# Optimization experiments

Measured on AMD Instinct MI355X. Metric: run time of the kernel, lower is better.

Reference implementation:

```python
import jax, jax.numpy as jnp
import numpy as np

B, H, W, C = 32, 56, 56, 192
HEADS = 6
WS = 7            # window size
SS = 3            # shift size
N = WS * WS       # tokens per window (49)
HID = 4 * C
EPS = 1e-5


def _rel_index():
    coords = np.stack(np.meshgrid(np.arange(WS), np.arange(WS), indexing='ij')).reshape(2, -1)
    rel = (coords[:, :, None] - coords[:, None, :]).transpose(1, 2, 0)
    rel[:, :, 0] += WS - 1
    rel[:, :, 1] += WS - 1
    rel[:, :, 0] *= 2 * WS - 1
    return rel.sum(-1)  # [N, N] int


def _attn_mask():
    # shift mask, identical to the torch construction; static -> numpy
    m = np.zeros((H, W))
    cnt = 0
    for hs in (slice(0, -WS), slice(-WS, -SS), slice(-SS, None)):
        for ws in (slice(0, -WS), slice(-WS, -SS), slice(-SS, None)):
            m[hs, ws] = cnt
            cnt += 1
    mw = m.reshape(H // WS, WS, W // WS, WS).transpose(0, 2, 1, 3).reshape(-1, N)  # [nW, N]
    diff = mw[:, None, :] - mw[:, :, None]
    return np.where(diff != 0, -100.0, 0.0).astype(np.float32)  # [nW, N, N]

REL_IDX = jnp.asarray(_rel_index())
ATTN_MASK = jnp.asarray(_attn_mask())


def setup_inputs() -> dict:
    key = jax.random.key(0)
    ks = jax.random.split(key, 16)
    s = 0.02
    return {
        'x': jax.random.normal(ks[0], (B, H, W, C), jnp.float32),
        'norm1_g': jnp.ones((C,), jnp.float32),
        'norm1_b': jnp.zeros((C,), jnp.float32),
        'qkv_w': jax.random.normal(ks[1], (C, 3 * C), jnp.float32) * s,
        'qkv_b': jnp.zeros((3 * C,), jnp.float32),
        'proj_w': jax.random.normal(ks[2], (C, C), jnp.float32) * s,
        'proj_b': jnp.zeros((C,), jnp.float32),
        'bias_table': jax.random.normal(ks[3], ((2 * WS - 1) ** 2, HEADS), jnp.float32) * s,
        'norm2_g': jnp.ones((C,), jnp.float32),
        'norm2_b': jnp.zeros((C,), jnp.float32),
        'fc1_w': jax.random.normal(ks[4], (C, HID), jnp.float32) * s,
        'fc1_b': jnp.zeros((HID,), jnp.float32),
        'fc2_w': jax.random.normal(ks[5], (HID, C), jnp.float32) * s,
        'fc2_b': jnp.zeros((C,), jnp.float32),
    }


def _ln(x, g, b):
    mu = jnp.mean(x, -1, keepdims=True)
    var = jnp.var(x, -1, keepdims=True)
    return (x - mu) * jax.lax.rsqrt(var + EPS) * g + b


def _partition(x):
    # [B,H,W,C] -> [B*nW, N, C]
    return x.reshape(B, H // WS, WS, W // WS, WS, C).transpose(0, 1, 3, 2, 4, 5).reshape(-1, N, C)


def _reverse(w):
    # [B*nW, N, C] -> [B,H,W,C]
    return w.reshape(B, H // WS, W // WS, WS, WS, C).transpose(0, 1, 3, 2, 4, 5).reshape(B, H, W, C)


def reference(x, norm1_g, norm1_b, qkv_w, qkv_b, proj_w, proj_b, bias_table,
              norm2_g, norm2_b, fc1_w, fc1_b, fc2_w, fc2_b):
    hd = C // HEADS
    scale = hd ** -0.5
    sc = x
    h = _ln(x, norm1_g, norm1_b)
    h = jnp.roll(h, (-SS, -SS), (1, 2))
    xw = _partition(h)                                  # [B_, N, C]
    B_ = xw.shape[0]
    qkv = (xw @ qkv_w + qkv_b).reshape(B_, N, 3, HEADS, hd).transpose(2, 0, 3, 1, 4)
    q, k, v = qkv[0], qkv[1], qkv[2]                    # [B_, H, N, hd]
    attn = jnp.einsum('bhnd,bhmd->bhnm', q * scale, k)  # [B_, H, N, N]
    bias = bias_table[REL_IDX.reshape(-1)].reshape(N, N, HEADS).transpose(2, 0, 1)
    attn = attn + bias[None]
    nW = (H // WS) * (W // WS)
    attn = attn.reshape(B, nW, HEADS, N, N) + ATTN_MASK[None, :, None]
    attn = jax.nn.softmax(attn.reshape(-1, HEADS, N, N), axis=-1)
    out = jnp.einsum('bhnm,bhmd->bhnd', attn, v).transpose(0, 2, 1, 3).reshape(B_, N, C)
    out = out @ proj_w + proj_b
    h = _reverse(out)
    h = jnp.roll(h, (SS, SS), (1, 2))
    y = sc + h
    m = _ln(y, norm2_g, norm2_b)
    mlp = jax.nn.gelu(m @ fc1_w + fc1_b, approximate=False) @ fc2_w + fc2_b
    return y + mlp
```

## Files before the change

kernel.cpp:

```cpp
#include <hip/hip_runtime.h>
#include <hip/hip_bf16.h>

typedef __hip_bfloat16 bf16;
typedef float f32x4 __attribute__((ext_vector_type(4)));
typedef short bf16x8 __attribute__((ext_vector_type(8)));
typedef short short4v __attribute__((ext_vector_type(4)));
typedef unsigned int u32;

#define NTOK 100352
#define CC 192
#define HIDN 768

__device__ __forceinline__ float b2f(unsigned short u) {
    union { unsigned int u32v; float f; } x; x.u32v = ((unsigned int)u) << 16; return x.f;
}
__device__ __forceinline__ unsigned short f2b(float f) {
    union { float f; unsigned int u; } x; x.f = f;
    unsigned int r = x.u + 0x7FFF + ((x.u >> 16) & 1);
    return (unsigned short)(r >> 16);
}
__device__ __forceinline__ float gelu_f(float x) {
    return x / (1.0f + __expf(-1.702f * x));
}

typedef __attribute__((address_space(1))) const unsigned char gas_u8;
typedef __attribute__((address_space(3))) unsigned char las_u8;
__device__ __forceinline__ void gload_lds16(const void* g, void* l) {
    __builtin_amdgcn_global_load_lds((gas_u8*)g, (las_u8*)l, 16, 0, 0);
}

__global__ void transpose_k(const float* __restrict__ src, bf16* __restrict__ dst, int R, int C) {
    int idx = blockIdx.x * 256 + threadIdx.x;
    if (idx >= R * C) return;
    int r = idx / C, c = idx % C;
    dst[(size_t)c * R + r] = __float2bfloat16(src[idx]);
}

__global__ void bm_k(const float* __restrict__ btab, float* __restrict__ bm) {
    int idx = blockIdx.x * 256 + threadIdx.x;
    if (idx >= 98304) return;
    int reg = idx & 3, lane = (idx >> 2) & 63, tile = (idx >> 8) & 15;
    int rest = idx >> 12, h = rest % 6, cls = rest / 6;
    int mt = tile >> 2, nt = tile & 3;
    int kk = mt * 16 + (lane >> 4) * 4 + reg;
    int q  = nt * 16 + (lane & 15);
    float v;
    if (kk >= 49 || q >= 49) v = -1e9f;
    else {
        int i1 = q / 7, j1 = q % 7, i2 = kk / 7, j2 = kk % 7;
        v = btab[((i1 - i2 + 6) * 13 + (j1 - j2 + 6)) * 6 + h];
        int hb7 = cls >> 1, wb7 = cls & 1;
        int r1 = (hb7 ? (i1 < 4 ? 1 : 2) : 0) * 3 + (wb7 ? (j1 < 4 ? 1 : 2) : 0);
        int r2 = (hb7 ? (i2 < 4 ? 1 : 2) : 0) * 3 + (wb7 ? (j2 < 4 ? 1 : 2) : 0);
        if (r1 != r2) v -= 100.0f;
    }
    bm[idx] = v;
}

template<bool GATHER>
__global__ __launch_bounds__(256) void ln_k(const float* __restrict__ src,
                                            const float* __restrict__ gamma,
                                            const float* __restrict__ beta,
                                            bf16* __restrict__ dst) {
    int wave = threadIdx.x >> 6, lane = threadIdx.x & 63;
    int t = blockIdx.x * 4 + wave;
    size_t srow;
    if (GATHER) {
        int w = t / 49, n = t % 49;
        int b = w >> 6, wl = w & 63, hb = wl >> 3, wb = wl & 7;
        int i = n / 7, j = n % 7;
        int sh = hb * 7 + i + 3; if (sh >= 56) sh -= 56;
        int sw = wb * 7 + j + 3; if (sw >= 56) sw -= 56;
        srow = ((size_t)(b * 56 + sh) * 56 + sw) * CC;
    } else {
        srow = (size_t)t * CC;
    }
    float v[4];
    int c = lane * 4;
    float sum = 0.f, sq = 0.f;
    if (lane < 48) {
        f32x4 d = *(const f32x4*)(src + srow + c);
        #pragma unroll
        for (int q = 0; q < 4; ++q) { v[q] = d[q]; sum += v[q]; sq += v[q] * v[q]; }
    }
    #pragma unroll
    for (int off = 1; off < 64; off <<= 1) { sum += __shfl_xor(sum, off); sq += __shfl_xor(sq, off); }
    float mu = sum * (1.0f / 192.0f);
    float var = sq * (1.0f / 192.0f) - mu * mu;
    float rstd = rsqrtf(var + 1e-5f);
    if (lane < 48) {
        f32x4 gg = *(const f32x4*)(gamma + c);
        f32x4 bb = *(const f32x4*)(beta + c);
        short4v o;
        #pragma unroll
        for (int q = 0; q < 4; ++q) {
            float val = (v[q] - mu) * rstd * gg[q] + bb[q];
            o[q] = (short)f2b(val);
        }
        *(short4v*)(dst + (size_t)t * CC + c) = o;
    }
}

template<int EPI>
__device__ __forceinline__ void epilogue(
    f32x4 (&acc)[4][2], int tm0, int tn0, int w0, int w1, int lane, int N,
    const float* __restrict__ bias, bf16* __restrict__ outb, float* __restrict__ outf,
    const float* __restrict__ xres, const float* __restrict__ yin)
{
    const int r16 = lane & 15, q4 = (lane >> 4) * 4;
    #pragma unroll
    for (int mt = 0; mt < 4; ++mt) {
        int mm = tm0 + w1 * 64 + mt * 16 + r16;
        size_t rowbase;
        if (EPI == 1) {
            int ww = mm / 49, nn = mm % 49;
            int b_ = ww >> 6, wl = ww & 63, hb = wl >> 3, wb = wl & 7;
            int i = nn / 7, j = nn % 7;
            int oh = hb * 7 + i + 3; if (oh >= 56) oh -= 56;
            int ow = wb * 7 + j + 3; if (ow >= 56) ow -= 56;
            rowbase = ((size_t)(b_ * 56 + oh) * 56 + ow) * CC;
        } else {
            rowbase = (size_t)mm * N;
        }
        #pragma unroll
        for (int nt = 0; nt < 2; ++nt) {
            int col = tn0 + w0 * 32 + nt * 16 + q4;
            f32x4 bv = *(const f32x4*)(bias + col);
            f32x4 v;
            #pragma unroll
            for (int r = 0; r < 4; ++r) v[r] = acc[mt][nt][r] + bv[r];
            if (EPI == 1) {
                f32x4 xr = *(const f32x4*)(xres + rowbase + col);
                #pragma unroll
                for (int r = 0; r < 4; ++r) v[r] += xr[r];
                *(f32x4*)(outf + rowbase + col) = v;
            } else if (EPI == 2) {
                short4v o;
                #pragma unroll
                for (int r = 0; r < 4; ++r) o[r] = (short)f2b(gelu_f(v[r]));
                *(short4v*)(outb + rowbase + col) = o;
            } else if (EPI == 3) {
                f32x4 yv = *(const f32x4*)(yin + rowbase + col);
                #pragma unroll
                for (int r = 0; r < 4; ++r) v[r] += yv[r];
                *(f32x4*)(outf + rowbase + col) = v;
            } else {
                size_t ob = ((size_t)(col >> 5) * NTOK + mm) * 32 + (col & 31);
                short4v o;
                #pragma unroll
                for (int r = 0; r < 4; ++r) o[r] = (short)f2b(v[r]);
                *(short4v*)(outb + ob) = o;
            }
        }
    }
}

template<int EPI, int NX>
__global__ __launch_bounds__(256) void gemm_ss(
    const bf16* __restrict__ X, const bf16* __restrict__ WT,
    const float* __restrict__ bias, int N,
    bf16* __restrict__ outb, float* __restrict__ outf,
    const float* __restrict__ xres, const float* __restrict__ yin)
{
    constexpr int K = 192;
    __shared__ bf16 As[3][128 * 64];
    const int tid = threadIdx.x;
    const int w = tid >> 6, lane = tid & 63;
    const int w0 = w & 1, w1 = w >> 1;

    const u32 nwg = NX * 784;
    u32 bid = blockIdx.y * NX + blockIdx.x;
    bid = (bid & 7) * (nwg >> 3) + (bid >> 3);
    const int tn0 = (int)(bid % NX) * 64;
    const int tm0 = (int)(bid / NX) * 128;

    const int r16 = lane & 15, g8 = (lane >> 4) * 8;

    const bf16* gW0 = WT + (size_t)(tn0 + w0 * 32 + r16) * K + g8;
    const bf16* gW1 = gW0 + 16 * K;
    bf16x8 wreg[3][2][2];
    #pragma unroll
    for (int t = 0; t < 3; ++t)
        #pragma unroll
        for (int k32 = 0; k32 < 2; ++k32) {
            wreg[t][k32][0] = *(const bf16x8*)(gW0 + t * 64 + k32 * 32);
            wreg[t][k32][1] = *(const bf16x8*)(gW1 + t * 64 + k32 * 32);
        }

    const bf16* gA[4];
    #pragma unroll
    for (int j = 0; j < 4; ++j) {
        int c = (w * 4 + j) * 64 + lane;
        int l = c ^ ((c >> 3) & 7);
        gA[j] = X + (size_t)(tm0 + (c >> 3)) * K + (l & 7) * 8;
    }
    #pragma unroll
    for (int t = 0; t < 3; ++t)
        #pragma unroll
        for (int j = 0; j < 4; ++j)
            gload_lds16(gA[j] + (t << 6), (char*)&As[t][0] + (size_t)(w * 4 + j) * 1024);
    __syncthreads();

    f32x4 acc[4][2] = {};
    #pragma unroll
    for (int t = 0; t < 3; ++t) {
        const char* ab = (const char*)&As[t][0];
        #pragma unroll
        for (int k32 = 0; k32 < 2; ++k32) {
            int kcolb = k32 * 64 + g8 * 2;
            bf16x8 xf[4];
            #pragma unroll
            for (int m = 0; m < 4; ++m) {
                int row = w1 * 64 + m * 16 + r16;
                int byte = row * 128 + kcolb;
                xf[m] = *(const bf16x8*)(ab + (byte ^ ((row & 7) << 4)));
            }
            #pragma unroll
            for (int m = 0; m < 4; ++m)
                #pragma unroll
                for (int n = 0; n < 2; ++n)
                    acc[m][n] = __builtin_amdgcn_mfma_f32_16x16x32_bf16(wreg[t][k32][n], xf[m], acc[m][n], 0, 0, 0);
        }
    }
    epilogue<EPI>(acc, tm0, tn0, w0, w1, lane, N, bias, outb, outf, xres, yin);
}

template<int EPI, int NX>
__global__ __launch_bounds__(256) void gemm_db(
    const bf16* __restrict__ X, const bf16* __restrict__ WT,
    const float* __restrict__ bias, int K, int N,
    bf16* __restrict__ outb, float* __restrict__ outf,
    const float* __restrict__ xres, const float* __restrict__ yin)
{
    __shared__ bf16 As[2][128 * 64];
    __shared__ bf16 Bs[2][64 * 64];
    const int tid = threadIdx.x;
    const int w = tid >> 6, lane = tid & 63;
    const int w0 = w & 1, w1 = w >> 1;

    const u32 nwg = NX * 784;
    u32 bid = blockIdx.y * NX + blockIdx.x;
    bid = (bid & 7) * (nwg >> 3) + (bid >> 3);
    const int tn0 = (int)(bid % NX) * 64;
    const int tm0 = (int)(bid / NX) * 128;

    const int r16 = lane & 15, g8 = (lane >> 4) * 8;

    const bf16* gA[4];
    const bf16* gB[2];
    #pragma unroll
    for (int j = 0; j < 4; ++j) {
        int c = (w * 4 + j) * 64 + lane;
        int l = c ^ ((c >> 3) & 7);
        gA[j] = X + (size_t)(tm0 + (c >> 3)) * K + (l & 7) * 8;
    }
    #pragma unroll
    for (int j = 0; j < 2; ++j) {
        int c = (w * 2 + j) * 64 + lane;
        int l = c ^ ((c >> 3) & 7);
        gB[j] = WT + (size_t)(tn0 + (c >> 3)) * K + (l & 7) * 8;
    }
    auto stage = [&](int buf, int kk) {
        #pragma unroll
        for (int j = 0; j < 4; ++j)
            gload_lds16(gA[j] + kk, (char*)&As[buf][0] + (size_t)(w * 4 + j) * 1024);
        #pragma unroll
        for (int j = 0; j < 2; ++j)
            gload_lds16(gB[j] + kk, (char*)&Bs[buf][0] + (size_t)(w * 2 + j) * 1024);
    };

    f32x4 acc[4][2] = {};
    const int nt = K >> 6;
    stage(0, 0);
    __syncthreads();
    for (int t = 0; t < nt; ++t) {
        int buf = t & 1;
        if (t + 1 < nt) stage(buf ^ 1, (t + 1) << 6);
        const char* ab = (const char*)&As[buf][0];
        const char* bb_ = (const char*)&Bs[buf][0];
        #pragma unroll
        for (int k32 = 0; k32 < 2; ++k32) {
            int kcolb = k32 * 64 + g8 * 2;
            bf16x8 xf[4], wf[2];
            #pragma unroll
            for (int m = 0; m < 4; ++m) {
                int row = w1 * 64 + m * 16 + r16;
                int byte = row * 128 + kcolb;
                xf[m] = *(const bf16x8*)(ab + (byte ^ ((row & 7) << 4)));
            }
            #pragma unroll
            for (int n = 0; n < 2; ++n) {
                int row = w0 * 32 + n * 16 + r16;
                int byte = row * 128 + kcolb;
                wf[n] = *(const bf16x8*)(bb_ + (byte ^ ((row & 7) << 4)));
            }
            #pragma unroll
            for (int m = 0; m < 4; ++m)
                #pragma unroll
                for (int n = 0; n < 2; ++n)
                    acc[m][n] = __builtin_amdgcn_mfma_f32_16x16x32_bf16(wf[n], xf[m], acc[m][n], 0, 0, 0);
        }
        __syncthreads();
    }
    epilogue<EPI>(acc, tm0, tn0, w0, w1, lane, N, bias, outb, outf, xres, yin);
}

__global__ __launch_bounds__(384) void attn_m(const bf16* __restrict__ qkv,
                                              const float* __restrict__ bm,
                                              bf16* __restrict__ out)
{
    __shared__ char Pl[6][8192];
    __shared__ char Vt[6][4096];
    const int w = blockIdx.x;
    const int h = threadIdx.x >> 6, l = threadIdx.x & 63;
    const int w49 = w * 49;
    const int wl = w & 63;
    const int cls = (((wl >> 3) == 7) ? 2 : 0) + (((wl & 7) == 7) ? 1 : 0);
    const int hi8 = (l >> 4) * 8, lo = l & 15;

    {
        const bf16* vbase = qkv + ((size_t)(12 + h) * NTOK + w49) * 32;
        #pragma unroll
        for (int it = 0; it < 4; ++it) {
            int c = it * 64 + l;
            int kk = c >> 2, off = (c & 3) * 8;
            bf16x8 v = {};
            if (c < 196) v = *(const bf16x8*)(vbase + kk * 32 + off);
            #pragma unroll
            for (int j = 0; j < 8; ++j) {
                int d = off + j;
                int byte = (d * 128 + kk * 2) ^ ((d & 7) << 4);
                *(bf16*)(&Vt[h][0] + byte) = ((const bf16*)&v)[j];
            }
        }
    }

    const bf16* qb = qkv + ((size_t)h * NTOK + w49) * 32 + hi8;
    const bf16* kb = qkv + ((size_t)(6 + h) * NTOK + w49) * 32 + hi8;
    bf16x8 af[4], bf_[4];
    #pragma unroll
    for (int mt = 0; mt < 4; ++mt) af[mt] = *(const bf16x8*)(kb + (size_t)(mt * 16 + lo) * 32);
    #pragma unroll
    for (int ntt = 0; ntt < 4; ++ntt) bf_[ntt] = *(const bf16x8*)(qb + (size_t)(ntt * 16 + lo) * 32);
    f32x4 acc[4][4] = {};
    #pragma unroll
    for (int mt = 0; mt < 4; ++mt)
        #pragma unroll
        for (int ntt = 0; ntt < 4; ++ntt)
            acc[mt][ntt] = __builtin_amdgcn_mfma_f32_16x16x32_bf16(af[mt], bf_[ntt], acc[mt][ntt], 0, 0, 0);

    const float scale = 0.17677669529663689f;
    const float* bmb = bm + ((size_t)(cls * 6 + h) << 4) * 256;
    #pragma unroll
    for (int mt = 0; mt < 4; ++mt)
        #pragma unroll
        for (int ntt = 0; ntt < 4; ++ntt) {
            f32x4 bmv = *(const f32x4*)(bmb + (mt * 4 + ntt) * 256 + l * 4);
            #pragma unroll
            for (int r = 0; r < 4; ++r) acc[mt][ntt][r] = acc[mt][ntt][r] * scale + bmv[r];
        }

    float inv[4], mx[4];
    #pragma unroll
    for (int ntt = 0; ntt < 4; ++ntt) {
        float m_ = -1e30f;
        #pragma unroll
        for (int mt = 0; mt < 4; ++mt)
            #pragma unroll
            for (int r = 0; r < 4; ++r) m_ = fmaxf(m_, acc[mt][ntt][r]);
        m_ = fmaxf(m_, __shfl_xor(m_, 16));
        m_ = fmaxf(m_, __shfl_xor(m_, 32));
        mx[ntt] = m_;
    }
    #pragma unroll
    for (int ntt = 0; ntt < 4; ++ntt) {
        float s_ = 0.f;
        #pragma unroll
        for (int mt = 0; mt < 4; ++mt)
            #pragma unroll
            for (int r = 0; r < 4; ++r) {
                float e = __expf(acc[mt][ntt][r] - mx[ntt]);
                acc[mt][ntt][r] = e;
                s_ += e;
            }
        s_ += __shfl_xor(s_, 16);
        s_ += __shfl_xor(s_, 32);
        inv[ntt] = 1.0f / s_;
    }

    #pragma unroll
    for (int mt = 0; mt < 4; ++mt)
        #pragma unroll
        for (int ntt = 0; ntt < 4; ++ntt)
            #pragma unroll
            for (int rp = 0; rp < 4; rp += 2) {
                u32 pk = (u32)f2b(acc[mt][ntt][rp]) | ((u32)f2b(acc[mt][ntt][rp + 1]) << 16);
                int kk = mt * 16 + (l >> 4) * 4 + rp;
                int q  = ntt * 16 + lo;
                int byte = (q * 128 + kk * 2) ^ ((q & 7) << 4);
                *(u32*)(&Pl[h][0] + byte) = pk;
            }

    f32x4 o[4][2] = {};
    #pragma unroll
    for (int ks = 0; ks < 2; ++ks) {
        int kb_ = (ks * 32 + hi8) * 2;
        bf16x8 pa[4], vb[2];
        #pragma unroll
        for (int qt = 0; qt < 4; ++qt) {
            int row = qt * 16 + lo;
            pa[qt] = *(const bf16x8*)(&Pl[h][0] + ((row * 128 + kb_) ^ ((row & 7) << 4)));
        }
        #pragma unroll
        for (int dt = 0; dt < 2; ++dt) {
            int row = dt * 16 + lo;
            vb[dt] = *(const bf16x8*)(&Vt[h][0] + ((row * 128 + kb_) ^ ((row & 7) << 4)));
        }
        #pragma unroll
        for (int qt = 0; qt < 4; ++qt)
            #pragma unroll
            for (int dt = 0; dt < 2; ++dt)
                o[qt][dt] = __builtin_amdgcn_mfma_f32_16x16x32_bf16(pa[qt], vb[dt], o[qt][dt], 0, 0, 0);
    }

    #pragma unroll
    for (int qt = 0; qt < 4; ++qt)
        #pragma unroll
        for (int r = 0; r < 4; ++r) {
            int qrow = (l >> 4) * 4 + r;
            float iv = __shfl(inv[qt], qrow);
            int q = qt * 16 + qrow;
            if (q < 49) {
                size_t ob = (size_t)(w49 + q) * CC + h * 32 + lo;
                out[ob]      = __float2bfloat16(o[qt][0][r] * iv);
                out[ob + 16] = __float2bfloat16(o[qt][1][r] * iv);
            }
        }
}

extern "C" void kernel_launch(void* const* d_in, const int* in_sizes, int n_in,
                              void* d_out, int out_size, void* d_ws, size_t ws_size,
                              hipStream_t stream) {
    const float* x      = (const float*)d_in[0];
    const float* n1g    = (const float*)d_in[1];
    const float* n1b    = (const float*)d_in[2];
    const float* qkv_w  = (const float*)d_in[3];
    const float* qkv_b  = (const float*)d_in[4];
    const float* proj_w = (const float*)d_in[5];
    const float* proj_b = (const float*)d_in[6];
    const float* btab   = (const float*)d_in[7];
    const float* n2g    = (const float*)d_in[8];
    const float* n2b    = (const float*)d_in[9];
    const float* fc1_w  = (const float*)d_in[10];
    const float* fc1_b  = (const float*)d_in[11];
    const float* fc2_w  = (const float*)d_in[12];
    const float* fc2_b  = (const float*)d_in[13];

    char* ws = (char*)d_ws;
    const size_t XW_OFF  = 0;
    const size_t QKV_OFF = 38535168;
    const size_t ATT_OFF = 154140672;
    const size_t WT_OFF  = 192675840;
    const size_t BM_OFF  = 193560576;
    if (ws_size < 193953792ull) return;

    bf16* xw   = (bf16*)(ws + XW_OFF);
    bf16* mbuf = (bf16*)(ws + XW_OFF);
    bf16* qkvb = (bf16*)(ws + QKV_OFF);
    bf16* attb = (bf16*)(ws + ATT_OFF);
    bf16* hidb = (bf16*)(ws + QKV_OFF);
    float* yf  = (float*)d_out;
    bf16* wt   = (bf16*)(ws + WT_OFF);
    float* bmt = (float*)(ws + BM_OFF);
    bf16* qkv_wT  = wt;
    bf16* proj_wT = wt + 110592;
    bf16* fc1_wT  = wt + 147456;
    bf16* fc2_wT  = wt + 294912;

    transpose_k<<<dim3(432), 256, 0, stream>>>(qkv_w, qkv_wT, 192, 576);
    transpose_k<<<dim3(144), 256, 0, stream>>>(proj_w, proj_wT, 192, 192);
    transpose_k<<<dim3(576), 256, 0, stream>>>(fc1_w, fc1_wT, 192, 768);
    transpose_k<<<dim3(576), 256, 0, stream>>>(fc2_w, fc2_wT, 768, 192);
    bm_k<<<dim3(384), 256, 0, stream>>>(btab, bmt);

    ln_k<true><<<NTOK / 4, 256, 0, stream>>>(x, n1g, n1b, xw);

    gemm_ss<4, 9><<<dim3(9, 784), 256, 0, stream>>>(
        xw, qkv_wT, qkv_b, 576, qkvb, nullptr, nullptr, nullptr);
    attn_m<<<dim3(2048), 384, 0, stream>>>(qkvb, bmt, attb);
    gemm_ss<1, 3><<<dim3(3, 784), 256, 0, stream>>>(
        attb, proj_wT, proj_b, 192, nullptr, yf, x, nullptr);

    ln_k<false><<<NTOK / 4, 256, 0, stream>>>(yf, n2g, n2b, mbuf);

    gemm_ss<2, 12><<<dim3(12, 784), 256, 0, stream>>>(
        mbuf, fc1_wT, fc1_b, 768, hidb, nullptr, nullptr, nullptr);
    gemm_db<3, 3><<<dim3(3, 784), 256, 0, stream>>>(
        hidb, fc2_wT, fc2_b, 768, 192, nullptr, yf, nullptr, yf);
}
```

Before: 400.3 us.

## Fuse fc1, GELU and fc2 into one MLP kernel keeping hidden in LDS

New measurement: 498.1 us. +24.4%, slower.

```diff
diff --git a/kernel.cpp b/kernel.cpp
--- a/kernel.cpp
+++ b/kernel.cpp
@@ -134,16 +134,6 @@
                 #pragma unroll
                 for (int r = 0; r < 4; ++r) v[r] += xr[r];
                 *(f32x4*)(outf + rowbase + col) = v;
-            } else if (EPI == 2) {
-                short4v o;
-                #pragma unroll
-                for (int r = 0; r < 4; ++r) o[r] = (short)f2b(gelu_f(v[r]));
-                *(short4v*)(outb + rowbase + col) = o;
-            } else if (EPI == 3) {
-                f32x4 yv = *(const f32x4*)(yin + rowbase + col);
-                #pragma unroll
-                for (int r = 0; r < 4; ++r) v[r] += yv[r];
-                *(f32x4*)(outf + rowbase + col) = v;
             } else {
                 size_t ob = ((size_t)(col >> 5) * NTOK + mm) * 32 + (col & 31);
                 short4v o;
@@ -225,29 +215,25 @@
     epilogue<EPI>(acc, tm0, tn0, w0, w1, lane, N, bias, outb, outf, xres, yin);
 }
 
-template<int EPI, int NX>
-__global__ __launch_bounds__(256) void gemm_db(
-    const bf16* __restrict__ X, const bf16* __restrict__ WT,
-    const float* __restrict__ bias, int K, int N,
-    bf16* __restrict__ outb, float* __restrict__ outf,
-    const float* __restrict__ xres, const float* __restrict__ yin)
+__global__ __launch_bounds__(256) void mlp_k(
+    const bf16* __restrict__ X, const bf16* __restrict__ W1T,
+    const bf16* __restrict__ W2T,
+    const float* __restrict__ b1, const float* __restrict__ b2,
+    float* __restrict__ yio)
 {
-    __shared__ bf16 As[2][128 * 64];
-    __shared__ bf16 Bs[2][64 * 64];
+    constexpr int K = 192;
+    __shared__ bf16 As[3][128 * 64];
+    __shared__ char Hs[32768];
     const int tid = threadIdx.x;
     const int w = tid >> 6, lane = tid & 63;
     const int w0 = w & 1, w1 = w >> 1;
-
-    const u32 nwg = NX * 784;
-    u32 bid = blockIdx.y * NX + blockIdx.x;
-    bid = (bid & 7) * (nwg >> 3) + (bid >> 3);
-    const int tn0 = (int)(bid % NX) * 64;
-    const int tm0 = (int)(bid / NX) * 128;
-
-    const int r16 = lane & 15, g8 = (lane >> 4) * 8;
+    const int r16 = lane & 15, g8 = (lane >> 4) * 8, q4 = (lane >> 4) * 4;
+
+    u32 bid = blockIdx.x;
+    bid = (bid & 7) * 98 + (bid >> 3);
+    const int tm0 = (int)bid * 128;
 
     const bf16* gA[4];
-    const bf16* gB[2];
     #pragma unroll
     for (int j = 0; j < 4; ++j) {
         int c = (w * 4 + j) * 64 + lane;
@@ -255,54 +241,103 @@
         gA[j] = X + (size_t)(tm0 + (c >> 3)) * K + (l & 7) * 8;
     }
     #pragma unroll
-    for (int j = 0; j < 2; ++j) {
-        int c = (w * 2 + j) * 64 + lane;
-        int l = c ^ ((c >> 3) & 7);
-        gB[j] = WT + (size_t)(tn0 + (c >> 3)) * K + (l & 7) * 8;
-    }
-    auto stage = [&](int buf, int kk) {
+    for (int t = 0; t < 3; ++t)
         #pragma unroll
         for (int j = 0; j < 4; ++j)
-            gload_lds16(gA[j] + kk, (char*)&As[buf][0] + (size_t)(w * 4 + j) * 1024);
-        #pragma unroll
-        for (int j = 0; j < 2; ++j)
-            gload_lds16(gB[j] + kk, (char*)&Bs[buf][0] + (size_t)(w * 2 + j) * 1024);
-    };
-
-    f32x4 acc[4][2] = {};
-    const int nt = K >> 6;
-    stage(0, 0);
+            gload_lds16(gA[j] + (t << 6), (char*)&As[t][0] + (size_t)(w * 4 + j) * 1024);
     __syncthreads();
-    for (int t = 0; t < nt; ++t) {
-        int buf = t & 1;
-        if (t + 1 < nt) stage(buf ^ 1, (t + 1) << 6);
-        const char* ab = (const char*)&As[buf][0];
-        const char* bb_ = (const char*)&Bs[buf][0];
-        #pragma unroll
-        for (int k32 = 0; k32 < 2; ++k32) {
+
+    f32x4 acc2[4][6] = {};
+
+    #pragma unroll 1
+    for (int s = 0; s < 6; ++s) {
+        f32x4 acc1[4][4] = {};
+        const bf16* w1b = W1T + (size_t)(s * 128 + w0 * 64 + r16) * K + g8;
+        #pragma unroll
+        for (int t = 0; t < 3; ++t) {
+            const char* ab = (const char*)&As[t][0];
+            #pragma unroll
+            for (int k32 = 0; k32 < 2; ++k32) {
+                int kg = t * 64 + k32 * 32;
+                int kcolb = k32 * 64 + g8 * 2;
+                bf16x8 wf[4], xf[4];
+                #pragma unroll
+                for (int n = 0; n < 4; ++n)
+                    wf[n] = *(const bf16x8*)(w1b + (size_t)(n * 16) * K + kg);
+                #pragma unroll
+                for (int m = 0; m < 4; ++m) {
+                    int row = w1 * 64 + m * 16 + r16;
+                    int byte = row * 128 + kcolb;
+                    xf[m] = *(const bf16x8*)(ab + (byte ^ ((row & 7) << 4)));
+                }
+                #pragma unroll
+                for (int m = 0; m < 4; ++m)
+                    #pragma unroll
+                    for (int n = 0; n < 4; ++n)
+                        acc1[m][n] = __builtin_amdgcn_mfma_f32_16x16x32_bf16(wf[n], xf[m], acc1[m][n], 0, 0, 0);
+            }
+        }
+        #pragma unroll
+        for (int m = 0; m < 4; ++m) {
+            int mloc = w1 * 64 + m * 16 + r16;
+            #pragma unroll
+            for (int n = 0; n < 4; ++n) {
+                int n1loc = w0 * 64 + n * 16 + q4;
+                f32x4 bv = *(const f32x4*)(b1 + s * 128 + n1loc);
+                u32 p0, p1;
+                {
+                    float v0 = gelu_f(acc1[m][n][0] + bv[0]);
+                    float v1 = gelu_f(acc1[m][n][1] + bv[1]);
+                    float v2 = gelu_f(acc1[m][n][2] + bv[2]);
+                    float v3 = gelu_f(acc1[m][n][3] + bv[3]);
+                    p0 = (u32)f2b(v0) | ((u32)f2b(v1) << 16);
+                    p1 = (u32)f2b(v2) | ((u32)f2b(v3) << 16);
+                }
+                int byte = (mloc * 256 + n1loc * 2) ^ ((mloc & 7) << 4);
+                *(u32*)(&Hs[0] + byte) = p0;
+                *(u32*)(&Hs[0] + byte + 4) = p1;
+            }
+        }
+        __syncthreads();
+
+        const bf16* w2b = W2T + (size_t)(w0 * 96 + r16) * HIDN + s * 128 + g8;
+        #pragma unroll
+        for (int k32 = 0; k32 < 4; ++k32) {
             int kcolb = k32 * 64 + g8 * 2;
-            bf16x8 xf[4], wf[2];
+            bf16x8 wf[6], hf[4];
+            #pragma unroll
+            for (int n = 0; n < 6; ++n)
+                wf[n] = *(const bf16x8*)(w2b + (size_t)(n * 16) * HIDN + k32 * 32);
             #pragma unroll
             for (int m = 0; m < 4; ++m) {
                 int row = w1 * 64 + m * 16 + r16;
-                int byte = row * 128 + kcolb;
-                xf[m] = *(const bf16x8*)(ab + (byte ^ ((row & 7) << 4)));
-            }
-            #pragma unroll
-            for (int n = 0; n < 2; ++n) {
-                int row = w0 * 32 + n * 16 + r16;
-                int byte = row * 128 + kcolb;
-                wf[n] = *(const bf16x8*)(bb_ + (byte ^ ((row & 7) << 4)));
+                int byte = row * 256 + kcolb;
+                hf[m] = *(const bf16x8*)(&Hs[0] + (byte ^ ((row & 7) << 4)));
             }
             #pragma unroll
             for (int m = 0; m < 4; ++m)
                 #pragma unroll
-                for (int n = 0; n < 2; ++n)
-                    acc[m][n] = __builtin_amdgcn_mfma_f32_16x16x32_bf16(wf[n], xf[m], acc[m][n], 0, 0, 0);
+                for (int n = 0; n < 6; ++n)
+                    acc2[m][n] = __builtin_amdgcn_mfma_f32_16x16x32_bf16(wf[n], hf[m], acc2[m][n], 0, 0, 0);
         }
         __syncthreads();
     }
-    epilogue<EPI>(acc, tm0, tn0, w0, w1, lane, N, bias, outb, outf, xres, yin);
+
+    #pragma unroll
+    for (int m = 0; m < 4; ++m) {
+        int mm = tm0 + w1 * 64 + m * 16 + r16;
+        size_t rowbase = (size_t)mm * CC;
+        #pragma unroll
+        for (int n = 0; n < 6; ++n) {
+            int col = w0 * 96 + n * 16 + q4;
+            f32x4 bv = *(const f32x4*)(b2 + col);
+            f32x4 yv = *(const f32x4*)(yio + rowbase + col);
+            f32x4 v;
+            #pragma unroll
+            for (int r = 0; r < 4; ++r) v[r] = acc2[m][n][r] + bv[r] + yv[r];
+            *(f32x4*)(yio + rowbase + col) = v;
+        }
+    }
 }
 
 __global__ __launch_bounds__(384) void attn_m(const bf16* __restrict__ qkv,
@@ -468,7 +503,6 @@
     bf16* mbuf = (bf16*)(ws + XW_OFF);
     bf16* qkvb = (bf16*)(ws + QKV_OFF);
     bf16* attb = (bf16*)(ws + ATT_OFF);
-    bf16* hidb = (bf16*)(ws + QKV_OFF);
     float* yf  = (float*)d_out;
     bf16* wt   = (bf16*)(ws + WT_OFF);
     float* bmt = (float*)(ws + BM_OFF);
@@ -493,8 +527,6 @@
 
     ln_k<false><<<NTOK / 4, 256, 0, stream>>>(yf, n2g, n2b, mbuf);
 
-    gemm_ss<2, 12><<<dim3(12, 784), 256, 0, stream>>>(
-        mbuf, fc1_wT, fc1_b, 768, hidb, nullptr, nullptr, nullptr);
-    gemm_db<3, 3><<<dim3(3, 784), 256, 0, stream>>>(
-        hidb, fc2_wT, fc2_b, 768, 192, nullptr, yf, nullptr, yf);
-}
+    mlp_k<<<dim3(784), 256, 0, stream>>>(
+        mbuf, fc1_wT, fc2_wT, fc1_b, fc2_b, yf);
+}
```
